# Optimization experiments

Hardware: AMD Instinct MI355X
Metric: run time of the kernel (lower is better)

Reference implementation:

```python
import jax, jax.numpy as jnp
from jax import lax
import numpy as np

D_MODEL, D_STATE, D_CONV, EXPAND = 512, 16, 4, 2
D_INNER = EXPAND * D_MODEL
B_SZ, SEQ = 16, 2048


def setup_inputs() -> dict:
    key = jax.random.key(0)
    ks = jax.random.split(key, 8)
    s = 0.02
    x = jax.random.normal(ks[0], (B_SZ, SEQ, D_MODEL), jnp.float32)
    W_in = jax.random.normal(ks[1], (2 * D_INNER, D_MODEL), jnp.float32) * s
    conv_w = jax.random.normal(ks[2], (D_INNER, 1, D_CONV), jnp.float32) * s
    conv_b = jnp.zeros((D_INNER,), jnp.float32)
    W_x = jax.random.normal(ks[3], (2 * D_STATE, D_INNER), jnp.float32) * s
    W_dt = jax.random.normal(ks[4], (D_INNER, D_INNER), jnp.float32) * s
    b_dt = jnp.zeros((D_INNER,), jnp.float32)
    # A_log = -logspace(log10(0.001), log10(1.0), d_state), exactly as in source
    A_log = jnp.asarray(-np.logspace(np.log10(0.001), 0.0, D_STATE), jnp.float32)
    D = jnp.ones((D_INNER,), jnp.float32) * 0.1
    W_out = jax.random.normal(ks[5], (D_MODEL, D_INNER), jnp.float32) * s
    ln_g = jnp.ones((D_MODEL,), jnp.float32)
    ln_b = jnp.zeros((D_MODEL,), jnp.float32)
    return dict(x=x, W_in=W_in, conv_w=conv_w, conv_b=conv_b, W_x=W_x,
                W_dt=W_dt, b_dt=b_dt, A_log=A_log, D=D, W_out=W_out,
                ln_g=ln_g, ln_b=ln_b)


def _selective_scan(u, delta, A, B, C, Dp):
    # u, delta: [b, s, di]; B, C: [b, s, ds]; A: [ds]; Dp: [di]
    def step(state, inp):
        d_t, u_t, B_t, C_t = inp            # [b,di],[b,di],[b,ds],[b,ds]
        dA = jnp.exp(jnp.clip(d_t[:, :, None] * A[None, None, :], -5.0, 5.0))
        dBu = (d_t * u_t)[:, :, None] * B_t[:, None, :]
        state = dA * state + dBu            # [b,di,ds]
        y_t = jnp.einsum('bds,bs->bd', state, C_t)
        return state, y_t

    b = u.shape[0]
    init = jnp.zeros((b, D_INNER, D_STATE), u.dtype)
    xs = (delta.transpose(1, 0, 2), u.transpose(1, 0, 2),
          B.transpose(1, 0, 2), C.transpose(1, 0, 2))
    _, ys = lax.scan(step, init, xs)        # [s, b, di]
    return ys.transpose(1, 0, 2) + u * Dp


def reference(x, W_in, conv_w, conv_b, W_x, W_dt, b_dt, A_log, D, W_out, ln_g, ln_b):
    x = jnp.clip(x, -10.0, 10.0)
    x_and_res = x @ W_in.T                  # [b, s, 2*di]
    x_p, res = jnp.split(x_and_res, 2, axis=-1)
    # causal depthwise conv1d (left pad d_conv-1, truncate to seq_len)
    xc = lax.conv_general_dilated(
        x_p.transpose(0, 2, 1), conv_w, window_strides=(1,),
        padding=[(D_CONV - 1, 0)], dimension_numbers=('NCH', 'OIH', 'NCH'),
        feature_group_count=D_INNER)
    xc = (xc + conv_b[None, :, None]).transpose(0, 2, 1)  # [b, s, di]
    xc = jax.nn.silu(xc)
    ssm = xc @ W_x.T                        # [b, s, 2*ds]
    Bm, Cm = jnp.split(ssm, 2, axis=-1)
    dt = xc @ W_dt.T + b_dt                 # [b, s, di]
    y = _selective_scan(xc, dt, A_log, Bm, Cm, D)
    y = y * jax.nn.silu(res)
    out = y @ W_out.T + x
    # LayerNorm (eps=1e-5)
    mu = out.mean(-1, keepdims=True)
    var = ((out - mu) ** 2).mean(-1, keepdims=True)
    return (out - mu) * lax.rsqrt(var + 1e-5) * ln_g + ln_b
```

## Files before the change

### kernel.cpp

```cpp
#include <hip/hip_runtime.h>
#include <hip/hip_bf16.h>
#include <math.h>

#define B_SZ 16
#define SEQ 2048
#define D_MODEL 512
#define D_INNER 1024
#define D_STATE 16
#define D_CONV 4
#define NSEG 64
#define SEGLEN (SEQ / NSEG)
#define LOG2E 1.44269504f

typedef __attribute__((ext_vector_type(8))) short short8;
typedef __attribute__((ext_vector_type(4))) float f32x4;
typedef const __attribute__((address_space(1))) void* gas_ptr;
typedef __attribute__((address_space(3))) void* las_ptr;

__device__ __forceinline__ float bf2f(unsigned int bits16) {
    union { unsigned int i; float f; } v; v.i = bits16 << 16; return v.f;
}
__device__ __forceinline__ unsigned short f2bf(float f) {
    union { float f; unsigned int i; } v; v.f = f;
    unsigned int r = v.i + 0x7FFFu + ((v.i >> 16) & 1u);
    return (unsigned short)(r >> 16);
}
__device__ __forceinline__ void async_g2l(const void* g, void* l) {
    __builtin_amdgcn_global_load_lds((gas_ptr)g, (las_ptr)l, 16, 0, 0);
}
__device__ __forceinline__ float fast_exp2(float x) { return __builtin_amdgcn_exp2f(x); }
__device__ __forceinline__ float fast_rcp(float x)  { return __builtin_amdgcn_rcpf(x); }
__device__ __forceinline__ float clamp3(float x, float lo, float hi) {
    return __builtin_amdgcn_fmed3f(x, lo, hi);
}
__device__ __forceinline__ float silu(float x) {
    return x * fast_rcp(1.f + fast_exp2(-x * LOG2E));
}

__global__ __launch_bounds__(256) void cast_bf16(
    const float4* __restrict__ in, ushort4* __restrict__ out, int n4, int do_clip)
{
    int i = blockIdx.x * 256 + threadIdx.x;
    if (i >= n4) return;
    float4 v = in[i];
    if (do_clip) {
        v.x = clamp3(v.x, -10.f, 10.f);
        v.y = clamp3(v.y, -10.f, 10.f);
        v.z = clamp3(v.z, -10.f, 10.f);
        v.w = clamp3(v.w, -10.f, 10.f);
    }
    ushort4 o;
    o.x = f2bf(v.x); o.y = f2bf(v.y); o.z = f2bf(v.z); o.w = f2bf(v.w);
    out[i] = o;
}

__global__ __launch_bounds__(256) void gemm_bf16(
    const unsigned short* __restrict__ A, const unsigned short* __restrict__ Bw,
    void* __restrict__ C, int K, int ldc, int nbn_shift,
    const float* __restrict__ bias,
    const float* __restrict__ add, int ldadd, int clip_add, int out_bf16)
{
    __shared__ unsigned short As[2][128][32];
    __shared__ unsigned short Bs[2][128][32];
    const int h = blockIdx.x;
    const int xk = h & 7;
    const int qb = h >> 3;
    const int bn = (qb & ((1 << nbn_shift) - 1)) * 128;
    const int bm = ((qb >> nbn_shift) * 8 + xk) * 128;
    const int tid = threadIdx.x;
    const int wv = tid >> 6;
    const int l  = tid & 63;
    const int lr = l >> 2;
    const int lc = l & 3;
    const int wm = (wv >> 1) * 64;
    const int wn = (wv & 1) * 64;
    const int r16 = l & 15;
    const int q   = l >> 4;
    const int gsw = (lc - ((lr >> 1) & 3)) & 3;
    const int ssw = ((q + ((r16 >> 1) & 3)) & 3) * 8;

    f32x4 acc[4][4];
    #pragma unroll
    for (int i = 0; i < 4; i++)
        #pragma unroll
        for (int j = 0; j < 4; j++)
            acc[i][j] = (f32x4){0.f, 0.f, 0.f, 0.f};

#define STAGE(kk, bb) { \
        const int k0_ = (kk) * 32; \
        _Pragma("unroll") \
        for (int p_ = 0; p_ < 2; p_++) { \
            const int row_ = wv * 32 + p_ * 16 + lr; \
            async_g2l((const char*)A + (((size_t)(bm + row_)) * K + k0_ + gsw * 8) * 2, \
                      (char*)&As[bb][0][0] + (wv * 32 + p_ * 16) * 64); \
            async_g2l((const char*)Bw + (((size_t)(bn + row_)) * K + k0_ + gsw * 8) * 2, \
                      (char*)&Bs[bb][0][0] + (wv * 32 + p_ * 16) * 64); \
        } }

    const int nk = K >> 5;
    STAGE(0, 0);
    __syncthreads();

    for (int kk = 0; kk < nk; kk++) {
        const int cur = kk & 1;
        if (kk + 1 < nk) STAGE(kk + 1, cur ^ 1);

        short8 af[4], bfv[4];
        #pragma unroll
        for (int i = 0; i < 4; i++) {
            af[i]  = *(const short8*)&As[cur][wm + i * 16 + r16][ssw];
            bfv[i] = *(const short8*)&Bs[cur][wn + i * 16 + r16][ssw];
        }
        #pragma unroll
        for (int i = 0; i < 4; i++)
            #pragma unroll
            for (int j = 0; j < 4; j++)
                acc[i][j] = __builtin_amdgcn_mfma_f32_16x16x32_bf16(
                    af[i], bfv[j], acc[i][j], 0, 0, 0);
        __syncthreads();
    }
#undef STAGE

    #pragma unroll
    for (int i = 0; i < 4; i++) {
        #pragma unroll
        for (int rr = 0; rr < 4; rr++) {
            int m = bm + wm + i * 16 + q * 4 + rr;
            #pragma unroll
            for (int j = 0; j < 4; j++) {
                int n = bn + wn + j * 16 + r16;
                float v = acc[i][j][rr];
                if (bias) v += bias[n];
                if (add) {
                    float a = add[(size_t)m * ldadd + n];
                    if (clip_add) a = clamp3(a, -10.f, 10.f);
                    v += a;
                }
                if (out_bf16)
                    ((unsigned short*)C)[(size_t)m * ldc + n] = f2bf(v);
                else
                    ((float*)C)[(size_t)m * ldc + n] = v;
            }
        }
    }
}

__global__ __launch_bounds__(256) void gemm_bc(
    const unsigned short* __restrict__ A, const unsigned short* __restrict__ Bw,
    float* __restrict__ C)
{
    const int tid = threadIdx.x;
    const int wv  = tid >> 6;
    const int l   = tid & 63;
    const int r16 = l & 15;
    const int q   = l >> 4;
    const int row0 = blockIdx.x * 64 + wv * 16;

    const unsigned short* ap  = A  + (size_t)(row0 + r16) * 1024 + q * 8;
    const unsigned short* bp0 = Bw + (size_t)r16 * 1024 + q * 8;
    const unsigned short* bp1 = Bw + (size_t)(16 + r16) * 1024 + q * 8;

    f32x4 acc0 = {0.f, 0.f, 0.f, 0.f}, acc1 = {0.f, 0.f, 0.f, 0.f};
    #pragma unroll 4
    for (int k = 0; k < 1024; k += 32) {
        short8 af = *(const short8*)(ap + k);
        short8 b0 = *(const short8*)(bp0 + k);
        short8 b1 = *(const short8*)(bp1 + k);
        acc0 = __builtin_amdgcn_mfma_f32_16x16x32_bf16(af, b0, acc0, 0, 0, 0);
        acc1 = __builtin_amdgcn_mfma_f32_16x16x32_bf16(af, b1, acc1, 0, 0, 0);
    }
    #pragma unroll
    for (int rr = 0; rr < 4; rr++) {
        int m = row0 + q * 4 + rr;
        C[(size_t)m * 32 + r16]      = acc0[rr];
        C[(size_t)m * 32 + 16 + r16] = acc1[rr];
    }
}

__global__ __launch_bounds__(256) void conv_silu(
    const unsigned short* __restrict__ xp, const float* __restrict__ cw,
    const float* __restrict__ cb, unsigned short* __restrict__ xc)
{
    int idx = blockIdx.x * 256 + threadIdx.x;
    int c4 = (idx & 255) << 2;
    int bt = idx >> 8;
    int t  = bt & (SEQ - 1);

    float4 acc = *(const float4*)(cb + c4);
    float4 w0 = *(const float4*)(cw + (c4 + 0) * 4);
    float4 w1 = *(const float4*)(cw + (c4 + 1) * 4);
    float4 w2 = *(const float4*)(cw + (c4 + 2) * 4);
    float4 w3 = *(const float4*)(cw + (c4 + 3) * 4);

    #pragma unroll
    for (int k = 0; k < D_CONV; k++) {
        int tt = t - (D_CONV - 1) + k;
        if (tt >= 0) {
            ushort4 xv = *(const ushort4*)(xp + (size_t)(bt - (D_CONV - 1) + k) * 2048 + c4);
            acc.x += bf2f(xv.x) * ((const float*)&w0)[k];
            acc.y += bf2f(xv.y) * ((const float*)&w1)[k];
            acc.z += bf2f(xv.z) * ((const float*)&w2)[k];
            acc.w += bf2f(xv.w) * ((const float*)&w3)[k];
        }
    }
    ushort4 o;
    o.x = f2bf(silu(acc.x));
    o.y = f2bf(silu(acc.y));
    o.z = f2bf(silu(acc.z));
    o.w = f2bf(silu(acc.w));
    *(ushort4*)(xc + (size_t)bt * 1024 + c4) = o;
}

__global__ __launch_bounds__(64, 4) void scan_phaseA(
    const unsigned short* __restrict__ xpres, const float* __restrict__ BC,
    const unsigned short* __restrict__ xc, const float* __restrict__ A_log,
    float* __restrict__ stA, float* __restrict__ prA)
{
    __shared__ float bc_lds[SEGLEN][32];
    const int bx = blockIdx.x;
    const int seg = bx & (NSEG - 1);
    const int dg  = (bx >> 6) & 15;
    const int b   = bx >> 10;
    if (seg == NSEG - 1) return;
    const int lane = threadIdx.x;
    const int d = dg * 64 + lane;
    const float CL = 5.f * LOG2E;

    const size_t rowbase = (size_t)b * SEQ + (size_t)seg * SEGLEN;
    const float* BCp = BC + rowbase * 32;

    #pragma unroll
    for (int c = 0; c < 4; c++)
        async_g2l(BCp + c * 256 + lane * 4,
                  (char*)&bc_lds[0][0] + c * 1024 + lane * 16);

    float A2[16];
    #pragma unroll
    for (int n = 0; n < 16; n++) A2[n] = A_log[n] * LOG2E;

    const unsigned short* dtp = xpres + rowbase * 2048 + d;
    const unsigned short* up  = xc + rowbase * 1024 + d;

    float st[16] = {};
    float se[16] = {};
    unsigned short dta[4], dtb[4], ua[4], ub[4];

#define LOADGA(g, dt_, u_) { \
        _Pragma("unroll") for (int jj = 0; jj < 4; ++jj) { \
            const int t_ = (g) * 4 + jj; \
            dt_[jj] = dtp[(size_t)t_ * 2048]; \
            u_[jj]  = up[(size_t)t_ * 1024]; \
        } }

#define COMPGA(g, dt_, u_) { \
        _Pragma("unroll") for (int jj = 0; jj < 4; ++jj) { \
            const int t_ = (g) * 4 + jj; \
            const float dtv_ = bf2f(dt_[jj]); \
            const float du_ = dtv_ * bf2f(u_[jj]); \
            float Bv_[16]; \
            _Pragma("unroll") for (int n = 0; n < 4; ++n) \
                *(float4*)&Bv_[n * 4] = *(const float4*)&bc_lds[t_][n * 4]; \
            _Pragma("unroll") for (int n = 0; n < 16; ++n) { \
                const float e_ = clamp3(dtv_ * A2[n], -CL, CL); \
                se[n] += e_; \
                st[n] = fast_exp2(e_) * st[n] + du_ * Bv_[n]; \
            } } }

    LOADGA(0, dta, ua);
    __syncthreads();

    for (int g = 0; g < 8; g += 2) {
        LOADGA(g + 1, dtb, ub);
        COMPGA(g, dta, ua);
        if (g + 2 < 8) LOADGA(g + 2, dta, ua);
        COMPGA(g + 1, dtb, ub);
    }
#undef LOADGA
#undef COMPGA

    size_t o = (((size_t)b * NSEG + seg) * 1024 + d) * 16;
    #pragma unroll
    for (int n4 = 0; n4 < 4; n4++) {
        *(float4*)(stA + o + n4 * 4) = *(float4*)&st[n4 * 4];
        float4 pv;
        pv.x = fast_exp2(clamp3(se[n4 * 4 + 0], -115.41f, 115.41f));
        pv.y = fast_exp2(clamp3(se[n4 * 4 + 1], -115.41f, 115.41f));
        pv.z = fast_exp2(clamp3(se[n4 * 4 + 2], -115.41f, 115.41f));
        pv.w = fast_exp2(clamp3(se[n4 * 4 + 3], -115.41f, 115.41f));
        *(float4*)(prA + o + n4 * 4) = pv;
    }
}

__global__ __launch_bounds__(256) void scan_combine(
    float* __restrict__ stA, const float* __restrict__ prA, int total)
{
    int idx = blockIdx.x * 256 + threadIdx.x;
    if (idx >= total) return;
    int dn = idx & 16383;
    int b  = idx >> 14;
    float prev = 0.f;
    #pragma unroll 4
    for (int s = 0; s < NSEG; s++) {
        size_t o = ((size_t)b * NSEG + s) * 16384 + dn;
        float a = stA[o], pr = prA[o];
        stA[o] = prev;
        prev = a + pr * prev;
    }
}

__global__ __launch_bounds__(64, 4) void scan_phaseC(
    const unsigned short* __restrict__ xpres, const float* __restrict__ BC,
    const unsigned short* __restrict__ xc, const float* __restrict__ A_log,
    const float* __restrict__ Dvec, const float* __restrict__ stIn,
    unsigned short* __restrict__ y_bf)
{
    __shared__ float bc_lds[SEGLEN][32];
    const int bx = blockIdx.x;
    const int seg = bx & (NSEG - 1);
    const int dg  = (bx >> 6) & 15;
    const int b   = bx >> 10;
    const int lane = threadIdx.x;
    const int d = dg * 64 + lane;
    const float CL = 5.f * LOG2E;

    const size_t rowbase = (size_t)b * SEQ + (size_t)seg * SEGLEN;
    const float* BCp = BC + rowbase * 32;

    #pragma unroll
    for (int c = 0; c < 4; c++)
        async_g2l(BCp + c * 256 + lane * 4,
                  (char*)&bc_lds[0][0] + c * 1024 + lane * 16);

    float A2[16];
    #pragma unroll
    for (int n = 0; n < 16; n++) A2[n] = A_log[n] * LOG2E;
    const float Dp = Dvec[d];

    const unsigned short* dtp  = xpres + rowbase * 2048 + d;
    const unsigned short* resp = xpres + rowbase * 2048 + 1024 + d;
    const unsigned short* up   = xc + rowbase * 1024 + d;
    unsigned short* yp = y_bf + rowbase * 1024 + d;

    float st[16];
    size_t o = (((size_t)b * NSEG + seg) * 1024 + d) * 16;
    #pragma unroll
    for (int n4 = 0; n4 < 4; n4++)
        *(float4*)&st[n4 * 4] = *(const float4*)(stIn + o + n4 * 4);

    unsigned short dta[4], dtb[4], ua[4], ub[4], ra[4], rb[4];

#define LOADGC(g, dt_, r_, u_) { \
        _Pragma("unroll") for (int jj = 0; jj < 4; ++jj) { \
            const int t_ = (g) * 4 + jj; \
            dt_[jj] = dtp[(size_t)t_ * 2048]; \
            r_[jj]  = resp[(size_t)t_ * 2048]; \
            u_[jj]  = up[(size_t)t_ * 1024]; \
        } }

#define COMPGC(g, dt_, r_, u_) { \
        _Pragma("unroll") for (int jj = 0; jj < 4; ++jj) { \
            const int t_ = (g) * 4 + jj; \
            const float dtv_ = bf2f(dt_[jj]); \
            const float uu_ = bf2f(u_[jj]); \
            const float du_ = dtv_ * uu_; \
            float V_[16]; \
            _Pragma("unroll") for (int n = 0; n < 4; ++n) \
                *(float4*)&V_[n * 4] = *(const float4*)&bc_lds[t_][n * 4]; \
            _Pragma("unroll") for (int n = 0; n < 16; ++n) { \
                const float e_ = clamp3(dtv_ * A2[n], -CL, CL); \
                st[n] = fast_exp2(e_) * st[n] + du_ * V_[n]; \
            } \
            _Pragma("unroll") for (int n = 0; n < 4; ++n) \
                *(float4*)&V_[n * 4] = *(const float4*)&bc_lds[t_][16 + n * 4]; \
            float y_ = 0.f; \
            _Pragma("unroll") for (int n = 0; n < 16; ++n) \
                y_ += st[n] * V_[n]; \
            const float outv_ = (y_ + uu_ * Dp) * silu(bf2f(r_[jj])); \
            yp[(size_t)t_ * 1024] = f2bf(outv_); \
        } }

    LOADGC(0, dta, ra, ua);
    __syncthreads();

    for (int g = 0; g < 8; g += 2) {
        LOADGC(g + 1, dtb, rb, ub);
        COMPGC(g, dta, ra, ua);
        if (g + 2 < 8) LOADGC(g + 2, dta, ra, ua);
        COMPGC(g + 1, dtb, rb, ub);
    }
#undef LOADGC
#undef COMPGC
}

__global__ __launch_bounds__(128) void ln_kernel(
    float* __restrict__ out, const float* __restrict__ g,
    const float* __restrict__ bta)
{
    const int row = blockIdx.x;
    float* p = out + (size_t)row * D_MODEL;
    const int tid = threadIdx.x;

    float4 v = ((const float4*)p)[tid];
    float s1 = v.x + v.y + v.z + v.w;
    float s2 = v.x * v.x + v.y * v.y + v.z * v.z + v.w * v.w;
    #pragma unroll
    for (int off = 32; off > 0; off >>= 1) {
        s1 += __shfl_xor(s1, off);
        s2 += __shfl_xor(s2, off);
    }
    __shared__ float r1[2], r2[2];
    if ((tid & 63) == 0) { r1[tid >> 6] = s1; r2[tid >> 6] = s2; }
    __syncthreads();
    s1 = r1[0] + r1[1];
    s2 = r2[0] + r2[1];

    const float mu  = s1 * (1.f / D_MODEL);
    const float var = s2 * (1.f / D_MODEL) - mu * mu;
    const float rstd = rsqrtf(var + 1e-5f);

    float4 gg = ((const float4*)g)[tid];
    float4 bb = ((const float4*)bta)[tid];
    float4 o;
    o.x = (v.x - mu) * rstd * gg.x + bb.x;
    o.y = (v.y - mu) * rstd * gg.y + bb.y;
    o.z = (v.z - mu) * rstd * gg.z + bb.z;
    o.w = (v.w - mu) * rstd * gg.w + bb.w;
    ((float4*)p)[tid] = o;
}

extern "C" void kernel_launch(void* const* d_in, const int* in_sizes, int n_in,
                              void* d_out, int out_size, void* d_ws, size_t ws_size,
                              hipStream_t stream)
{
    const float* x      = (const float*)d_in[0];
    const float* W_in   = (const float*)d_in[1];
    const float* conv_w = (const float*)d_in[2];
    const float* conv_b = (const float*)d_in[3];
    const float* W_x    = (const float*)d_in[4];
    const float* W_dt   = (const float*)d_in[5];
    const float* b_dt   = (const float*)d_in[6];
    const float* A_log  = (const float*)d_in[7];
    const float* Dv     = (const float*)d_in[8];
    const float* W_out  = (const float*)d_in[9];
    const float* ln_g   = (const float*)d_in[10];
    const float* ln_b   = (const float*)d_in[11];
    float* out = (float*)d_out;

    const size_t szWin  = (size_t)2048 * 512;
    const size_t szWdt  = (size_t)1024 * 1024;
    const size_t szWout = (size_t)512 * 1024;
    const size_t szWx   = (size_t)32 * 1024;
    char* p = (char*)d_ws;
    unsigned short* Wib  = (unsigned short*)p; p += szWin * 2;
    unsigned short* Wdtb = (unsigned short*)p; p += szWdt * 2;
    unsigned short* Wob  = (unsigned short*)p; p += szWout * 2;
    unsigned short* Wxb  = (unsigned short*)p; p += szWx * 2;
    const size_t fixed_bytes = (size_t)(p - (char*)d_ws);

    const size_t per_batch =
        (size_t)SEQ * 2048 * 2
      + (size_t)SEQ * 1024 * 2
      + (size_t)SEQ * 1024 * 2
      + (size_t)SEQ * 32 * 4
      + (size_t)2 * NSEG * 1024 * 16 * 4;
    int cb = 16;
    while (cb > 1 && fixed_bytes + (size_t)cb * per_batch > ws_size) cb >>= 1;
    const int Mc = cb * SEQ;

    unsigned short* xpres = (unsigned short*)p; p += (size_t)Mc * 2048 * 2;
    unsigned short* ybuf  = (unsigned short*)p; p += (size_t)Mc * 1024 * 2;
    unsigned short* x_bf  = ybuf;
    unsigned short* xc_bf = (unsigned short*)p; p += (size_t)Mc * 1024 * 2;
    float*          BCb   = (float*)p;          p += (size_t)Mc * 32 * 4;
    float*          stA   = (float*)p;          p += (size_t)cb * NSEG * 16384 * 4;
    float*          prA   = (float*)p;

    cast_bf16<<<(int)(szWin / 4 + 255) / 256, 256, 0, stream>>>((const float4*)W_in,  (ushort4*)Wib,  (int)(szWin / 4), 0);
    cast_bf16<<<(int)(szWdt / 4 + 255) / 256, 256, 0, stream>>>((const float4*)W_dt,  (ushort4*)Wdtb, (int)(szWdt / 4), 0);
    cast_bf16<<<(int)(szWout / 4 + 255) / 256, 256, 0, stream>>>((const float4*)W_out, (ushort4*)Wob, (int)(szWout / 4), 0);
    cast_bf16<<<(int)(szWx / 4 + 255) / 256, 256, 0, stream>>>((const float4*)W_x,   (ushort4*)Wxb,  (int)(szWx / 4), 0);

    for (int b0 = 0; b0 < B_SZ; b0 += cb) {
        const float* xk   = x   + (size_t)b0 * SEQ * D_MODEL;
        float*       outk = out + (size_t)b0 * SEQ * D_MODEL;

        cast_bf16<<<(Mc * 512 / 4) / 256, 256, 0, stream>>>(
            (const float4*)xk, (ushort4*)x_bf, Mc * 512 / 4, 1);

        gemm_bf16<<<(2048 / 128) * (Mc / 128), 256, 0, stream>>>(
            x_bf, Wib, xpres, 512, 2048, 4, nullptr, nullptr, 0, 0, 1);

        conv_silu<<<Mc, 256, 0, stream>>>(xpres, conv_w, conv_b, xc_bf);

        gemm_bc<<<Mc / 64, 256, 0, stream>>>(xc_bf, Wxb, BCb);

        gemm_bf16<<<(1024 / 128) * (Mc / 128), 256, 0, stream>>>(
            xc_bf, Wdtb, xpres, 1024, 2048, 3, b_dt, nullptr, 0, 0, 1);

        scan_phaseA<<<cb * NSEG * 16, 64, 0, stream>>>(xpres, BCb, xc_bf, A_log, stA, prA);
        scan_combine<<<(cb * 16384 + 255) / 256, 256, 0, stream>>>(stA, prA, cb * 16384);
        scan_phaseC<<<cb * NSEG * 16, 64, 0, stream>>>(xpres, BCb, xc_bf, A_log, Dv, stA, ybuf);

        gemm_bf16<<<(512 / 128) * (Mc / 128), 256, 0, stream>>>(
            ybuf, Wob, outk, 1024, 512, 2, nullptr, xk, 512, 1, 0);

        ln_kernel<<<Mc, 128, 0, stream>>>(outk, ln_g, ln_b);
    }
}
```

Measured before the change: 964.6 us.

## Triple-buffer GEMM loads and add 256x128 tile GEMM for input projections

Converts the GEMM main loop from double buffering with two syncthreads to a three-stage async LDS pipeline. Each iteration waits on vmcnt counters and uses a single barrier, and the prefetch runs two K-steps ahead. Adds a 512-thread gemm_big kernel with 256x128 tiles for the in-projection and dt projections, which raises reuse of the B operand per block. The cost is more LDS per block, and correctness now depends on the hand-counted vmcnt waits matching the number of issued loads.

```diff
diff --git a/kernel.cpp b/kernel.cpp
--- a/kernel.cpp
+++ b/kernel.cpp
@@ -36,6 +36,9 @@
 __device__ __forceinline__ float silu(float x) {
     return x * fast_rcp(1.f + fast_exp2(-x * LOG2E));
 }
+__device__ __forceinline__ void vm_wait0() { asm volatile("s_waitcnt vmcnt(0)" ::: "memory"); }
+__device__ __forceinline__ void vm_wait3() { asm volatile("s_waitcnt vmcnt(3)" ::: "memory"); }
+__device__ __forceinline__ void vm_wait4() { asm volatile("s_waitcnt vmcnt(4)" ::: "memory"); }
 
 __global__ __launch_bounds__(256) void cast_bf16(
     const float4* __restrict__ in, ushort4* __restrict__ out, int n4, int do_clip)
@@ -54,14 +57,111 @@
     out[i] = o;
 }
 
+__global__ __launch_bounds__(512, 4) void gemm_big(
+    const unsigned short* __restrict__ A, const unsigned short* __restrict__ Bw,
+    void* __restrict__ C, int K, int ldc, int nbn_shift,
+    const float* __restrict__ bias,
+    const float* __restrict__ add, int ldadd, int clip_add, int out_bf16)
+{
+    __shared__ unsigned short As[3][256][32];
+    __shared__ unsigned short Bs[3][128][32];
+    const int h = blockIdx.x;
+    const int xk = h & 7;
+    const int qb = h >> 3;
+    const int bn = (qb & ((1 << nbn_shift) - 1)) * 128;
+    const int bm = ((qb >> nbn_shift) * 8 + xk) * 256;
+    const int tid = threadIdx.x;
+    const int wv = tid >> 6;
+    const int l  = tid & 63;
+    const int lr = l >> 2;
+    const int lc = l & 3;
+    const int wm = (wv >> 1) * 64;
+    const int wn = (wv & 1) * 64;
+    const int r16 = l & 15;
+    const int q   = l >> 4;
+    const int gsw = (lc - ((lr >> 1) & 3)) & 3;
+    const int ssw = ((q + ((r16 >> 1) & 3)) & 3) * 8;
+
+    f32x4 acc[4][4];
+    #pragma unroll
+    for (int i = 0; i < 4; i++)
+        #pragma unroll
+        for (int j = 0; j < 4; j++)
+            acc[i][j] = (f32x4){0.f, 0.f, 0.f, 0.f};
+
+#define STAGEB(kk, bb) { \
+        const int k0_ = (kk) * 32; \
+        _Pragma("unroll") \
+        for (int p_ = 0; p_ < 2; p_++) { \
+            const int arow_ = wv * 32 + p_ * 16 + lr; \
+            async_g2l((const char*)A + (((size_t)(bm + arow_)) * K + k0_ + gsw * 8) * 2, \
+                      (char*)&As[bb][wv * 32 + p_ * 16][0]); \
+        } \
+        const int brow_ = wv * 16 + lr; \
+        async_g2l((const char*)Bw + (((size_t)(bn + brow_)) * K + k0_ + gsw * 8) * 2, \
+                  (char*)&Bs[bb][wv * 16][0]); \
+    }
+
+    const int nk = K >> 5;
+    STAGEB(0, 0);
+    STAGEB(1, 1);
+    int c0 = 0, c1 = 1, c2 = 2;
+
+    for (int kk = 0; kk < nk; kk++) {
+        if (kk + 1 < nk) vm_wait3(); else vm_wait0();
+        __builtin_amdgcn_s_barrier();
+
+        short8 af[4], bfv[4];
+        #pragma unroll
+        for (int i = 0; i < 4; i++) {
+            af[i]  = *(const short8*)&As[c0][wm + i * 16 + r16][ssw];
+            bfv[i] = *(const short8*)&Bs[c0][wn + i * 16 + r16][ssw];
+        }
+        if (kk + 2 < nk) STAGEB(kk + 2, c2);
+
+        #pragma unroll
+        for (int i = 0; i < 4; i++)
+            #pragma unroll
+            for (int j = 0; j < 4; j++)
+                acc[i][j] = __builtin_amdgcn_mfma_f32_16x16x32_bf16(
+                    af[i], bfv[j], acc[i][j], 0, 0, 0);
+
+        int t = c0; c0 = c1; c1 = c2; c2 = t;
+    }
+#undef STAGEB
+
+    #pragma unroll
+    for (int i = 0; i < 4; i++) {
+        #pragma unroll
+        for (int rr = 0; rr < 4; rr++) {
+            int m = bm + wm + i * 16 + q * 4 + rr;
+            #pragma unroll
+            for (int j = 0; j < 4; j++) {
+                int n = bn + wn + j * 16 + r16;
+                float v = acc[i][j][rr];
+                if (bias) v += bias[n];
+                if (add) {
+                    float a = add[(size_t)m * ldadd + n];
+                    if (clip_add) a = clamp3(a, -10.f, 10.f);
+                    v += a;
+                }
+                if (out_bf16)
+                    ((unsigned short*)C)[(size_t)m * ldc + n] = f2bf(v);
+                else
+                    ((float*)C)[(size_t)m * ldc + n] = v;
+            }
+        }
+    }
+}
+
 __global__ __launch_bounds__(256) void gemm_bf16(
     const unsigned short* __restrict__ A, const unsigned short* __restrict__ Bw,
     void* __restrict__ C, int K, int ldc, int nbn_shift,
     const float* __restrict__ bias,
     const float* __restrict__ add, int ldadd, int clip_add, int out_bf16)
 {
-    __shared__ unsigned short As[2][128][32];
-    __shared__ unsigned short Bs[2][128][32];
+    __shared__ unsigned short As[3][128][32];
+    __shared__ unsigned short Bs[3][128][32];
     const int h = blockIdx.x;
     const int xk = h & 7;
     const int qb = h >> 3;
@@ -92,32 +192,36 @@
         for (int p_ = 0; p_ < 2; p_++) { \
             const int row_ = wv * 32 + p_ * 16 + lr; \
             async_g2l((const char*)A + (((size_t)(bm + row_)) * K + k0_ + gsw * 8) * 2, \
-                      (char*)&As[bb][0][0] + (wv * 32 + p_ * 16) * 64); \
+                      (char*)&As[bb][wv * 32 + p_ * 16][0]); \
             async_g2l((const char*)Bw + (((size_t)(bn + row_)) * K + k0_ + gsw * 8) * 2, \
-                      (char*)&Bs[bb][0][0] + (wv * 32 + p_ * 16) * 64); \
+                      (char*)&Bs[bb][wv * 32 + p_ * 16][0]); \
         } }
 
     const int nk = K >> 5;
     STAGE(0, 0);
-    __syncthreads();
+    STAGE(1, 1);
+    int c0 = 0, c1 = 1, c2 = 2;
 
     for (int kk = 0; kk < nk; kk++) {
-        const int cur = kk & 1;
-        if (kk + 1 < nk) STAGE(kk + 1, cur ^ 1);
+        if (kk + 1 < nk) vm_wait4(); else vm_wait0();
+        __builtin_amdgcn_s_barrier();
 
         short8 af[4], bfv[4];
         #pragma unroll
         for (int i = 0; i < 4; i++) {
-            af[i]  = *(const short8*)&As[cur][wm + i * 16 + r16][ssw];
-            bfv[i] = *(const short8*)&Bs[cur][wn + i * 16 + r16][ssw];
+            af[i]  = *(const short8*)&As[c0][wm + i * 16 + r16][ssw];
+            bfv[i] = *(const short8*)&Bs[c0][wn + i * 16 + r16][ssw];
         }
+        if (kk + 2 < nk) STAGE(kk + 2, c2);
+
         #pragma unroll
         for (int i = 0; i < 4; i++)
             #pragma unroll
             for (int j = 0; j < 4; j++)
                 acc[i][j] = __builtin_amdgcn_mfma_f32_16x16x32_bf16(
                     af[i], bfv[j], acc[i][j], 0, 0, 0);
-        __syncthreads();
+
+        int t = c0; c0 = c1; c1 = c2; c2 = t;
     }
 #undef STAGE
 
@@ -487,21 +591,21 @@
         cast_bf16<<<(Mc * 512 / 4) / 256, 256, 0, stream>>>(
             (const float4*)xk, (ushort4*)x_bf, Mc * 512 / 4, 1);
 
-        gemm_bf16<<<(2048 / 128) * (Mc / 128), 256, 0, stream>>>(
+        gemm_big<<<16 * (Mc / 256), 512, 0, stream>>>(
             x_bf, Wib, xpres, 512, 2048, 4, nullptr, nullptr, 0, 0, 1);
 
         conv_silu<<<Mc, 256, 0, stream>>>(xpres, conv_w, conv_b, xc_bf);
 
         gemm_bc<<<Mc / 64, 256, 0, stream>>>(xc_bf, Wxb, BCb);
 
-        gemm_bf16<<<(1024 / 128) * (Mc / 128), 256, 0, stream>>>(
+        gemm_big<<<8 * (Mc / 256), 512, 0, stream>>>(
             xc_bf, Wdtb, xpres, 1024, 2048, 3, b_dt, nullptr, 0, 0, 1);
 
         scan_phaseA<<<cb * NSEG * 16, 64, 0, stream>>>(xpres, BCb, xc_bf, A_log, stA, prA);
         scan_combine<<<(cb * 16384 + 255) / 256, 256, 0, stream>>>(stA, prA, cb * 16384);
         scan_phaseC<<<cb * NSEG * 16, 64, 0, stream>>>(xpres, BCb, xc_bf, A_log, Dv, stA, ybuf);
 
-        gemm_bf16<<<(512 / 128) * (Mc / 128), 256, 0, stream>>>(
+        gemm_bf16<<<4 * (Mc / 128), 256, 0, stream>>>(
             ybuf, Wob, outk, 1024, 512, 2, nullptr, xk, 512, 1, 0);
 
         ln_kernel<<<Mc, 128, 0, stream>>>(outk, ln_g, ln_b);
```

Result: faster. 875.8 us (-9.2%).
